# Kernel tuning notes

Measured on AMD Instinct MI355X. Metric: run time of the kernel, lower is better.

The kernel has to match this reference:

```python
import jax, jax.numpy as jnp
import numpy as np

SEQ = 64      # len(features): number of timesteps for the (seq-major) LSTM
B = 40        # the expand(.., 40, ..) axis -> LSTM batch dim (batch_first=False)
IN = 8192 * 2 # 16384
H = 1024


def setup_inputs() -> dict:
    key = jax.random.key(0)
    k1, k2, k3, k4, k5 = jax.random.split(key, 5)
    s = 1.0 / np.sqrt(H)  # PyTorch LSTM init scale
    features = jax.random.normal(k1, (SEQ, IN), dtype=jnp.float32)
    w_ih = jax.random.uniform(k2, (4 * H, IN), jnp.float32, -s, s)
    w_hh = jax.random.uniform(k3, (4 * H, H), jnp.float32, -s, s)
    b_ih = jax.random.uniform(k4, (4 * H,), jnp.float32, -s, s)
    b_hh = jax.random.uniform(k5, (4 * H,), jnp.float32, -s, s)
    return {"features": features, "w_ih": w_ih, "w_hh": w_hh, "b_ih": b_ih, "b_hh": b_hh}


def reference(features, w_ih, w_hh, b_ih, b_hh):
    # features: [SEQ, IN]. The torch code expands each row to 40 identical
    # batch elements; since the input projection is identical across those
    # copies we compute it once per timestep and broadcast over B.
    xw = features @ w_ih.T + (b_ih + b_hh)  # [SEQ, 4H], hoisted big GEMM

    def step(carry, xw_t):
        h, c = carry                      # each [B, H]
        gates = xw_t[None, :] + h @ w_hh.T  # [B, 4H]
        i, f, g, o = jnp.split(gates, 4, axis=-1)  # PyTorch gate order i,f,g,o
        i = jax.nn.sigmoid(i)
        f = jax.nn.sigmoid(f)
        g = jnp.tanh(g)
        o = jax.nn.sigmoid(o)
        c = f * c + i * g
        h = o * jnp.tanh(c)
        return (h, c), h

    h0 = jnp.zeros((B, H), dtype=features.dtype)
    c0 = jnp.zeros((B, H), dtype=features.dtype)
    _, hs = jax.lax.scan(step, (h0, c0), xw)
    return hs  # [SEQ, B, H] == (seq_len, batch, hidden) as torch returns
```

## Files before the change

### kernel.cpp

```cpp
#include <hip/hip_runtime.h>
#include <hip/hip_bf16.h>
#include <math.h>

#define SEQ 64
#define IN_DIM 16384
#define H_DIM 1024
#define G4 4096
#define BATCH 40
#define NB_SCAN 64
#define NT_SCAN 1024

typedef short bf16x8 __attribute__((ext_vector_type(8)));
typedef float f32x4 __attribute__((ext_vector_type(4)));
typedef unsigned int uvec4 __attribute__((ext_vector_type(4)));
typedef unsigned int uvec2 __attribute__((ext_vector_type(2)));

#define OFF_AH   256
#define OFF_AL   (OFF_AH + (size_t)SEQ * IN_DIM / 2)
#define OFF_XW   (OFF_AL + (size_t)SEQ * IN_DIM / 2)
#define OFF_HS   (OFF_XW + (size_t)SEQ * G4)
#define OFF_PART (OFF_HS + (size_t)SEQ * H_DIM)

__global__ void zero_bar(unsigned* bar) { bar[threadIdx.x] = 0u; }

__global__ __launch_bounds__(256) void convert_a(const float* __restrict__ f,
                                                 unsigned* __restrict__ a_hi,
                                                 unsigned* __restrict__ a_lo) {
    const int i = blockIdx.x * 256 + threadIdx.x;
    uvec4 u = ((const uvec4*)f)[i];
    unsigned h0 = (u.x >> 16) | (u.y & 0xffff0000u);
    unsigned h1 = (u.z >> 16) | (u.w & 0xffff0000u);
    float l0 = __uint_as_float(u.x) - __uint_as_float(u.x & 0xffff0000u);
    float l1 = __uint_as_float(u.y) - __uint_as_float(u.y & 0xffff0000u);
    float l2 = __uint_as_float(u.z) - __uint_as_float(u.z & 0xffff0000u);
    float l3 = __uint_as_float(u.w) - __uint_as_float(u.w & 0xffff0000u);
    unsigned q0 = (__float_as_uint(l0) >> 16) | (__float_as_uint(l1) & 0xffff0000u);
    unsigned q1 = (__float_as_uint(l2) >> 16) | (__float_as_uint(l3) & 0xffff0000u);
    uvec2 hv; hv.x = h0; hv.y = h1;
    uvec2 lv; lv.x = q0; lv.y = q1;
    ((uvec2*)a_hi)[i] = hv;
    ((uvec2*)a_lo)[i] = lv;
}

__global__ __launch_bounds__(256, 2) void gemm_mfma(const float* __restrict__ w_ih,
                                                    const unsigned* __restrict__ a_hi,
                                                    const unsigned* __restrict__ a_lo,
                                                    float* __restrict__ part, int kspan) {
    const int tid = threadIdx.x;
    const int wv   = tid >> 6;
    const int lane = tid & 63;
    const int col  = lane & 15;
    const int kg   = lane >> 4;
    const int jbase = blockIdx.x * 64 + wv * 16 + col;
    const int k0base = blockIdx.y * kspan;

    const float* wrow = w_ih + (size_t)jbase * IN_DIM;

    f32x4 acc[4] = {};

    for (int k0 = k0base; k0 < k0base + kspan; k0 += 32) {
        const int kf = k0 + kg * 8;
        uvec4 u0 = *(const uvec4*)(wrow + kf);
        uvec4 u1 = *(const uvec4*)(wrow + kf + 4);
        uvec4 hb, lb;
        hb.x = (u0.x >> 16) | (u0.y & 0xffff0000u);
        hb.y = (u0.z >> 16) | (u0.w & 0xffff0000u);
        hb.z = (u1.x >> 16) | (u1.y & 0xffff0000u);
        hb.w = (u1.z >> 16) | (u1.w & 0xffff0000u);
        float f0 = __uint_as_float(u0.x) - __uint_as_float(u0.x & 0xffff0000u);
        float f1 = __uint_as_float(u0.y) - __uint_as_float(u0.y & 0xffff0000u);
        float f2 = __uint_as_float(u0.z) - __uint_as_float(u0.z & 0xffff0000u);
        float f3 = __uint_as_float(u0.w) - __uint_as_float(u0.w & 0xffff0000u);
        float f4 = __uint_as_float(u1.x) - __uint_as_float(u1.x & 0xffff0000u);
        float f5 = __uint_as_float(u1.y) - __uint_as_float(u1.y & 0xffff0000u);
        float f6 = __uint_as_float(u1.z) - __uint_as_float(u1.z & 0xffff0000u);
        float f7 = __uint_as_float(u1.w) - __uint_as_float(u1.w & 0xffff0000u);
        lb.x = (__float_as_uint(f0) >> 16) | (__float_as_uint(f1) & 0xffff0000u);
        lb.y = (__float_as_uint(f2) >> 16) | (__float_as_uint(f3) & 0xffff0000u);
        lb.z = (__float_as_uint(f4) >> 16) | (__float_as_uint(f5) & 0xffff0000u);
        lb.w = (__float_as_uint(f6) >> 16) | (__float_as_uint(f7) & 0xffff0000u);
        bf16x8 bhi = __builtin_bit_cast(bf16x8, hb);
        bf16x8 blo = __builtin_bit_cast(bf16x8, lb);

#pragma unroll
        for (int i = 0; i < 4; ++i) {
            const size_t aidx = (size_t)(i * 16 + col) * (IN_DIM / 2) + (kf >> 1);
            uvec4 ah = *(const uvec4*)(a_hi + aidx);
            uvec4 al = *(const uvec4*)(a_lo + aidx);
            bf16x8 ahv = __builtin_bit_cast(bf16x8, ah);
            bf16x8 alv = __builtin_bit_cast(bf16x8, al);
            acc[i] = __builtin_amdgcn_mfma_f32_16x16x32_bf16(ahv, bhi, acc[i], 0, 0, 0);
            acc[i] = __builtin_amdgcn_mfma_f32_16x16x32_bf16(alv, bhi, acc[i], 0, 0, 0);
            acc[i] = __builtin_amdgcn_mfma_f32_16x16x32_bf16(ahv, blo, acc[i], 0, 0, 0);
        }
    }
    float* pb = part + (size_t)blockIdx.y * (SEQ * G4);
#pragma unroll
    for (int i = 0; i < 4; ++i)
#pragma unroll
        for (int r = 0; r < 4; ++r) {
            const int trow = i * 16 + kg * 4 + r;
            pb[(size_t)trow * G4 + jbase] = acc[i][r];
        }
}

__global__ __launch_bounds__(256) void reduce_xw(const float* __restrict__ part,
                                                 const float* __restrict__ b_ih,
                                                 const float* __restrict__ b_hh,
                                                 float* __restrict__ xw, int KS) {
    const int idx = blockIdx.x * 256 + threadIdx.x;
    const int j = idx & (G4 - 1);
    float s = b_ih[j] + b_hh[j];
    for (int ks = 0; ks < KS; ++ks) s += part[(size_t)ks * (SEQ * G4) + idx];
    xw[idx] = s;
}

__global__ __launch_bounds__(NT_SCAN, 1) void lstm_scan(const float* __restrict__ xw,
                                                        const float* __restrict__ w_hh,
                                                        float* __restrict__ hs_c,
                                                        unsigned* __restrict__ bar) {
    const int tid = threadIdx.x;
    const int b = blockIdx.x;
    const int r = tid & 63;
    const int q = tid >> 6;
    const int g = r >> 4;
    const int jl = r & 15;
    const size_t grow = (size_t)g * H_DIM + (size_t)b * 16 + jl;

    float4 w[16];
    {
        const float4* wp = (const float4*)(w_hh + grow * H_DIM + q * 64);
#pragma unroll
        for (int m = 0; m < 16; ++m) w[m] = wp[m];
    }
#pragma unroll
    for (int m = 0; m < 16; ++m)
        asm volatile("" : "+v"(w[m].x), "+v"(w[m].y), "+v"(w[m].z), "+v"(w[m].w));

    __shared__ float h_lds[H_DIM];
    __shared__ float red[64][17];
    __shared__ float gate_lds[64];

    float c_reg = 0.f;

    for (int t = 0; t < SEQ; ++t) {
        float xwv = 0.f;
        if (tid < 64)
            xwv = xw[(size_t)t * G4 + (size_t)(tid >> 4) * H_DIM + b * 16 + (tid & 15)];
        float acc = 0.f;
        if (t > 0) {
            h_lds[tid] = __hip_atomic_load(hs_c + (size_t)(t - 1) * H_DIM + tid,
                                           __ATOMIC_RELAXED, __HIP_MEMORY_SCOPE_AGENT);
            __syncthreads();
#pragma unroll
            for (int m = 0; m < 16; ++m) {
                float4 h4 = *(const float4*)&h_lds[q * 64 + m * 4];
                acc += w[m].x * h4.x + w[m].y * h4.y + w[m].z * h4.z + w[m].w * h4.w;
            }
        }
        red[r][q] = acc;
        __syncthreads();
        if (tid < 64) {
            float s = 0.f;
#pragma unroll
            for (int qq = 0; qq < 16; ++qq) s += red[tid][qq];
            gate_lds[tid] = xwv + s;
        }
        __syncthreads();
        if (tid < 16) {
            float iv = gate_lds[tid];
            float fv = gate_lds[16 + tid];
            float gv = gate_lds[32 + tid];
            float ov = gate_lds[48 + tid];
            iv = 1.f / (1.f + expf(-iv));
            fv = 1.f / (1.f + expf(-fv));
            gv = tanhf(gv);
            ov = 1.f / (1.f + expf(-ov));
            c_reg = fv * c_reg + iv * gv;
            float hv = ov * tanhf(c_reg);
            __hip_atomic_store(hs_c + (size_t)t * H_DIM + b * 16 + tid, hv,
                               __ATOMIC_RELAXED, __HIP_MEMORY_SCOPE_AGENT);
        }
        if (t < SEQ - 1) {
            asm volatile("s_waitcnt vmcnt(0)" ::: "memory");
            if (tid == 0)
                __hip_atomic_store(bar + b, (unsigned)t + 1u,
                                   __ATOMIC_RELAXED, __HIP_MEMORY_SCOPE_AGENT);
            if (tid < 64) {
                const unsigned target = (unsigned)t + 1u;
                unsigned v = __hip_atomic_load(bar + tid, __ATOMIC_RELAXED,
                                               __HIP_MEMORY_SCOPE_AGENT);
                while (__all((int)(v >= target)) == 0) {
                    __builtin_amdgcn_s_sleep(1);
                    v = __hip_atomic_load(bar + tid, __ATOMIC_RELAXED,
                                          __HIP_MEMORY_SCOPE_AGENT);
                }
                asm volatile("" ::: "memory");
            }
            __syncthreads();
        }
    }
}

__global__ __launch_bounds__(256) void bcast_out(const float* __restrict__ hs_c,
                                                 float* __restrict__ out) {
    const int gi = blockIdx.x * 256 + threadIdx.x;
    const int t = gi / (BATCH * (H_DIM / 4));
    const int rem = gi - t * (BATCH * (H_DIM / 4));
    const int jq = rem & (H_DIM / 4 - 1);
    const float4 v = ((const float4*)hs_c)[t * (H_DIM / 4) + jq];
    ((float4*)out)[gi] = v;
}

extern "C" void kernel_launch(void* const* d_in, const int* in_sizes, int n_in,
                              void* d_out, int out_size, void* d_ws, size_t ws_size,
                              hipStream_t stream) {
    const float* features = (const float*)d_in[0];
    const float* w_ih     = (const float*)d_in[1];
    const float* w_hh     = (const float*)d_in[2];
    const float* b_ih     = (const float*)d_in[3];
    const float* b_hh     = (const float*)d_in[4];
    float* out = (float*)d_out;
    float* ws  = (float*)d_ws;

    unsigned* bar  = (unsigned*)d_ws;
    unsigned* a_hi = (unsigned*)(ws + OFF_AH);
    unsigned* a_lo = (unsigned*)(ws + OFF_AL);
    float* xw   = ws + OFF_XW;
    float* hs_c = ws + OFF_HS;
    float* part = ws + OFF_PART;

    int KS = 8;
    while (KS > 1 && (OFF_PART + (size_t)KS * SEQ * G4) * 4 > ws_size) KS >>= 1;
    const int kspan = IN_DIM / KS;

    zero_bar<<<1, 256, 0, stream>>>(bar);
    convert_a<<<(SEQ * IN_DIM / 4) / 256, 256, 0, stream>>>(features, a_hi, a_lo);
    gemm_mfma<<<dim3(G4 / 64, KS), 256, 0, stream>>>(w_ih, a_hi, a_lo, part, kspan);
    reduce_xw<<<(SEQ * G4) / 256, 256, 0, stream>>>(part, b_ih, b_hh, xw, KS);
    lstm_scan<<<NB_SCAN, NT_SCAN, 0, stream>>>(xw, w_hh, hs_c, bar);
    bcast_out<<<(SEQ * BATCH * H_DIM / 4) / 256, 256, 0, stream>>>(hs_c, out);
}
```

Baseline: 738.6 us.

## Replace grid barrier with per-element poison-flag polling on hidden state

Removes the per-step global barrier counter. The hidden-state buffer is pre-filled with a poison pattern, and each thread spins on its own h element until a real value appears. Values are stored with a +2 bias so that a valid h can never equal the poison pattern, and the bias is subtracted when reading and in the output broadcast. The block's own h slice is taken from LDS. The intent is to cut barrier round-trips and let blocks proceed as soon as their inputs land, at the cost of an extra poison kernel and reliance on per-word atomic visibility.

Measured after the change: 634.0 us. 14.2% less time.

```diff
diff --git a/kernel.cpp b/kernel.cpp
--- a/kernel.cpp
+++ b/kernel.cpp
@@ -9,6 +9,8 @@
 #define BATCH 40
 #define NB_SCAN 64
 #define NT_SCAN 1024
+#define POISON 0xAAAAAAAAu
+#define H_BIAS 2.0f
 
 typedef short bf16x8 __attribute__((ext_vector_type(8)));
 typedef float f32x4 __attribute__((ext_vector_type(4)));
@@ -21,7 +23,11 @@
 #define OFF_HS   (OFF_XW + (size_t)SEQ * G4)
 #define OFF_PART (OFF_HS + (size_t)SEQ * H_DIM)
 
-__global__ void zero_bar(unsigned* bar) { bar[threadIdx.x] = 0u; }
+__global__ __launch_bounds__(256) void poison_hs(unsigned* __restrict__ hs) {
+    const int i = blockIdx.x * 256 + threadIdx.x;
+    uvec4 p; p.x = POISON; p.y = POISON; p.z = POISON; p.w = POISON;
+    ((uvec4*)hs)[i] = p;
+}
 
 __global__ __launch_bounds__(256) void convert_a(const float* __restrict__ f,
                                                  unsigned* __restrict__ a_hi,
@@ -117,8 +123,7 @@
 
 __global__ __launch_bounds__(NT_SCAN, 1) void lstm_scan(const float* __restrict__ xw,
                                                         const float* __restrict__ w_hh,
-                                                        float* __restrict__ hs_c,
-                                                        unsigned* __restrict__ bar) {
+                                                        float* __restrict__ hs_c) {
     const int tid = threadIdx.x;
     const int b = blockIdx.x;
     const int r = tid & 63;
@@ -140,6 +145,10 @@
     __shared__ float h_lds[H_DIM];
     __shared__ float red[64][17];
     __shared__ float gate_lds[64];
+    __shared__ float h_own[16];
+
+    const unsigned* hs_u = (const unsigned*)hs_c;
+    const int my_src = tid >> 4;
 
     float c_reg = 0.f;
 
@@ -149,8 +158,17 @@
             xwv = xw[(size_t)t * G4 + (size_t)(tid >> 4) * H_DIM + b * 16 + (tid & 15)];
         float acc = 0.f;
         if (t > 0) {
-            h_lds[tid] = __hip_atomic_load(hs_c + (size_t)(t - 1) * H_DIM + tid,
-                                           __ATOMIC_RELAXED, __HIP_MEMORY_SCOPE_AGENT);
+            if (my_src == b) {
+                h_lds[tid] = h_own[tid & 15];
+            } else {
+                unsigned v = __hip_atomic_load(hs_u + (size_t)(t - 1) * H_DIM + tid,
+                                               __ATOMIC_RELAXED, __HIP_MEMORY_SCOPE_AGENT);
+                while (v == POISON) {
+                    v = __hip_atomic_load(hs_u + (size_t)(t - 1) * H_DIM + tid,
+                                          __ATOMIC_RELAXED, __HIP_MEMORY_SCOPE_AGENT);
+                }
+                h_lds[tid] = __uint_as_float(v) - H_BIAS;
+            }
             __syncthreads();
 #pragma unroll
             for (int m = 0; m < 16; ++m) {
@@ -178,27 +196,11 @@
             ov = 1.f / (1.f + expf(-ov));
             c_reg = fv * c_reg + iv * gv;
             float hv = ov * tanhf(c_reg);
-            __hip_atomic_store(hs_c + (size_t)t * H_DIM + b * 16 + tid, hv,
+            h_own[tid] = hv;
+            __hip_atomic_store(hs_c + (size_t)t * H_DIM + b * 16 + tid, hv + H_BIAS,
                                __ATOMIC_RELAXED, __HIP_MEMORY_SCOPE_AGENT);
         }
-        if (t < SEQ - 1) {
-            asm volatile("s_waitcnt vmcnt(0)" ::: "memory");
-            if (tid == 0)
-                __hip_atomic_store(bar + b, (unsigned)t + 1u,
-                                   __ATOMIC_RELAXED, __HIP_MEMORY_SCOPE_AGENT);
-            if (tid < 64) {
-                const unsigned target = (unsigned)t + 1u;
-                unsigned v = __hip_atomic_load(bar + tid, __ATOMIC_RELAXED,
-                                               __HIP_MEMORY_SCOPE_AGENT);
-                while (__all((int)(v >= target)) == 0) {
-                    __builtin_amdgcn_s_sleep(1);
-                    v = __hip_atomic_load(bar + tid, __ATOMIC_RELAXED,
-                                          __HIP_MEMORY_SCOPE_AGENT);
-                }
-                asm volatile("" ::: "memory");
-            }
-            __syncthreads();
-        }
+        __syncthreads();
     }
 }
 
@@ -208,7 +210,8 @@
     const int t = gi / (BATCH * (H_DIM / 4));
     const int rem = gi - t * (BATCH * (H_DIM / 4));
     const int jq = rem & (H_DIM / 4 - 1);
-    const float4 v = ((const float4*)hs_c)[t * (H_DIM / 4) + jq];
+    float4 v = ((const float4*)hs_c)[t * (H_DIM / 4) + jq];
+    v.x -= H_BIAS; v.y -= H_BIAS; v.z -= H_BIAS; v.w -= H_BIAS;
     ((float4*)out)[gi] = v;
 }
 
@@ -223,7 +226,6 @@
     float* out = (float*)d_out;
     float* ws  = (float*)d_ws;
 
-    unsigned* bar  = (unsigned*)d_ws;
     unsigned* a_hi = (unsigned*)(ws + OFF_AH);
     unsigned* a_lo = (unsigned*)(ws + OFF_AL);
     float* xw   = ws + OFF_XW;
@@ -234,10 +236,10 @@
     while (KS > 1 && (OFF_PART + (size_t)KS * SEQ * G4) * 4 > ws_size) KS >>= 1;
     const int kspan = IN_DIM / KS;
 
-    zero_bar<<<1, 256, 0, stream>>>(bar);
+    poison_hs<<<(SEQ * H_DIM / 4) / 256, 256, 0, stream>>>((unsigned*)hs_c);
     convert_a<<<(SEQ * IN_DIM / 4) / 256, 256, 0, stream>>>(features, a_hi, a_lo);
     gemm_mfma<<<dim3(G4 / 64, KS), 256, 0, stream>>>(w_ih, a_hi, a_lo, part, kspan);
     reduce_xw<<<(SEQ * G4) / 256, 256, 0, stream>>>(part, b_ih, b_hh, xw, KS);
-    lstm_scan<<<NB_SCAN, NT_SCAN, 0, stream>>>(xw, w_hh, hs_c, bar);
+    lstm_scan<<<NB_SCAN, NT_SCAN, 0, stream>>>(xw, w_hh, hs_c);
     bcast_out<<<(SEQ * BATCH * H_DIM / 4) / 256, 256, 0, stream>>>(hs_c, out);
 }
```
